# Kernel tuning notes

Hardware: AMD Instinct MI355X
Metric: run time of the kernel (lower is better)

## Reference

```python
import jax, jax.numpy as jnp
import numpy as np

W = 5           # input_instances
H = W // 2      # half_input_instances
N = 16384       # total ragged tokens (sum of lengths)
D = 1024        # hidden_dim


def setup_inputs() -> dict:
    key = jax.random.key(0)
    # 8 variable-length sequences summing to N
    lengths = np.array([1024, 3072, 2048, 4096, 512, 1536, 2560, 1536], dtype=np.int64)
    assert lengths.sum() == N
    x = jax.random.normal(key, (N, D), dtype=jnp.float32)
    return {"x": x, "lengths": jnp.asarray(lengths)}


def reference(x, lengths):
    # Equivalent to: per-sequence zero-pad by H on both sides, unfold window W stride 1,
    # concat, reshape to [N, D*W]. out[n, d*W + w] = padded_seq[t + w, d] where t is the
    # local position of token n, zero when t + w - H is out of the sequence.
    n, d = x.shape
    cum = jnp.cumsum(lengths)                 # [S] sequence end offsets
    starts = cum - lengths                    # [S] sequence start offsets
    pos = jnp.arange(n)                       # [N] global token index
    seg = jnp.searchsorted(cum, pos, side='right')  # [N] sequence id per token
    local = pos - starts[seg]                 # [N] local position within sequence
    seq_len = lengths[seg]                    # [N] length of owning sequence
    offs = jnp.arange(W) - H                  # [W] window offsets relative to center
    src_local = local[:, None] + offs[None, :]              # [N, W]
    valid = (src_local >= 0) & (src_local < seq_len[:, None])
    src = jnp.clip(src_local, 0, seq_len[:, None] - 1) + starts[seg][:, None]
    gathered = jnp.where(valid[:, :, None], x[src], jnp.zeros((), x.dtype))  # [N, W, D]
    # unfold layout is [N, D, W]; row-major flatten -> out[n, d*W + w]
    return jnp.transpose(gathered, (0, 2, 1)).reshape(n, d * W)
```

## Files before the change

kernel.cpp:

```cpp
#include <hip/hip_runtime.h>


#define WIN 5
#define HALF 2
#define DIM 1024
#define DV (DIM / 4)
#define OUTV (DV * WIN)
#define NSEQ 8
#define T 8
#define ROWS (T + 2 * HALF)

typedef float f32x4 __attribute__((ext_vector_type(4)));

__global__ __launch_bounds__(256) void inflate_kernel(
    const f32x4* __restrict__ x4,
    const int*   __restrict__ lengths,
    f32x4*       __restrict__ out4,
    int N)
{
    __shared__ float lds[ROWS * DIM];

    const int nb    = gridDim.x;
    const int chunk = nb >> 3;
    const int bid   = blockIdx.x;
    const int newb  = (bid & 7) * chunk + (bid >> 3);
    const int t0    = newb * T;

    const int g = threadIdx.x;

    f32x4* lds4 = (f32x4*)lds;
#pragma unroll
    for (int rr = 0; rr < ROWS; ++rr) {
        const int gr = t0 - HALF + rr;
        f32x4 v = (f32x4)0.f;
        if (gr >= 0 && gr < N) v = x4[(size_t)gr * DV + g];
        lds4[rr * DV + g] = v;
    }

    int Ls[NSEQ];
#pragma unroll
    for (int s = 0; s < NSEQ; ++s) Ls[s] = lengths[s];

    __syncthreads();

    const int wid  = g >> 6;
    const int lane = g & 63;

#pragma unroll
    for (int ti = 0; ti < 2; ++ti) {
        const int tt = wid * 2 + ti;
        const int n  = t0 + tt;

        int start = 0, end = N, acc = 0;
#pragma unroll
        for (int s = 0; s < NSEQ; ++s) {
            const int L = Ls[s];
            if (n >= acc && n < acc + L) { start = acc; end = acc + L; }
            acc += L;
        }
        int wlo = start - n + HALF; if (wlo < 0) wlo = 0;
        int whi = end - n + HALF - 1; if (whi > WIN - 1) whi = WIN - 1;

        const float* ldsbase = lds + tt * DIM;
        f32x4* dst = out4 + (size_t)n * OUTV;

        if (wlo == 0 && whi == WIN - 1) {
#pragma unroll
            for (int k = 0; k < OUTV / 64; ++k) {
                const unsigned j  = k * 64 + lane;
                const unsigned p0 = 4 * j;
                f32x4 o;
                { unsigned p = p0 + 0, d = p / WIN, w = p - d * WIN; o.x = ldsbase[w * DIM + d]; }
                { unsigned p = p0 + 1, d = p / WIN, w = p - d * WIN; o.y = ldsbase[w * DIM + d]; }
                { unsigned p = p0 + 2, d = p / WIN, w = p - d * WIN; o.z = ldsbase[w * DIM + d]; }
                { unsigned p = p0 + 3, d = p / WIN, w = p - d * WIN; o.w = ldsbase[w * DIM + d]; }
                __builtin_nontemporal_store(o, &dst[j]);
            }
        } else {
#pragma unroll
            for (int k = 0; k < OUTV / 64; ++k) {
                const unsigned j  = k * 64 + lane;
                const unsigned p0 = 4 * j;
                f32x4 o;
                { unsigned p = p0 + 0, d = p / WIN; int w = (int)(p - d * WIN);
                  o.x = (w >= wlo && w <= whi) ? ldsbase[w * DIM + d] : 0.f; }
                { unsigned p = p0 + 1, d = p / WIN; int w = (int)(p - d * WIN);
                  o.y = (w >= wlo && w <= whi) ? ldsbase[w * DIM + d] : 0.f; }
                { unsigned p = p0 + 2, d = p / WIN; int w = (int)(p - d * WIN);
                  o.z = (w >= wlo && w <= whi) ? ldsbase[w * DIM + d] : 0.f; }
                { unsigned p = p0 + 3, d = p / WIN; int w = (int)(p - d * WIN);
                  o.w = (w >= wlo && w <= whi) ? ldsbase[w * DIM + d] : 0.f; }
                __builtin_nontemporal_store(o, &dst[j]);
            }
        }
    }
}

extern "C" void kernel_launch(void* const* d_in, const int* in_sizes, int n_in,
                              void* d_out, int out_size, void* d_ws, size_t ws_size,
                              hipStream_t stream) {
    const float* x       = (const float*)d_in[0];
    const int*   lengths = (const int*)d_in[1];
    float*       out     = (float*)d_out;

    const int N = in_sizes[0] / DIM;

    dim3 grid(N / T), block(256);
    hipLaunchKernelGGL(inflate_kernel, grid, block, 0, stream,
                       (const f32x4*)x, lengths, (f32x4*)out, N);
}
```

Baseline: 72.28 us.

## Double token tile, split hidden dim in halves, load LDS via global_load_lds

Raises the tokens per block from 8 to 16, which shrinks the halo re-read overhead from 12/8 to 20/16 rows per block. To keep LDS size bounded, the hidden dimension is processed in two halves with a barrier between them. Input rows are loaded straight into LDS with the global_load_lds builtin, bypassing registers. Each wave now emits four output rows per half. The trade-off is half as many blocks, an extra synchronisation point, and no overlap between loading the second half and storing the first.

```diff
diff --git a/kernel.cpp b/kernel.cpp
--- a/kernel.cpp
+++ b/kernel.cpp
@@ -7,18 +7,27 @@
 #define DV (DIM / 4)
 #define OUTV (DV * WIN)
 #define NSEQ 8
-#define T 8
+#define T 16
 #define ROWS (T + 2 * HALF)
+#define HD (DIM / 2)
+#define HOUTV (OUTV / 2)
 
 typedef float f32x4 __attribute__((ext_vector_type(4)));
 
+__device__ inline void gload_lds16(const float* g, float* l) {
+    __builtin_amdgcn_global_load_lds(
+        (const __attribute__((address_space(1))) void*)g,
+        (__attribute__((address_space(3))) void*)l,
+        16, 0, 0);
+}
+
 __global__ __launch_bounds__(256) void inflate_kernel(
-    const f32x4* __restrict__ x4,
+    const float* __restrict__ x,
     const int*   __restrict__ lengths,
     f32x4*       __restrict__ out4,
     int N)
 {
-    __shared__ float lds[ROWS * DIM];
+    __shared__ float lds[ROWS * HD];
 
     const int nb    = gridDim.x;
     const int chunk = nb >> 3;
@@ -26,71 +35,84 @@
     const int newb  = (bid & 7) * chunk + (bid >> 3);
     const int t0    = newb * T;
 
-    const int g = threadIdx.x;
-
-    f32x4* lds4 = (f32x4*)lds;
-#pragma unroll
-    for (int rr = 0; rr < ROWS; ++rr) {
-        const int gr = t0 - HALF + rr;
-        f32x4 v = (f32x4)0.f;
-        if (gr >= 0 && gr < N) v = x4[(size_t)gr * DV + g];
-        lds4[rr * DV + g] = v;
-    }
+    const int g    = threadIdx.x;
+    const int wid  = g >> 6;
+    const int lane = g & 63;
 
     int Ls[NSEQ];
 #pragma unroll
     for (int s = 0; s < NSEQ; ++s) Ls[s] = lengths[s];
 
-    __syncthreads();
-
-    const int wid  = g >> 6;
-    const int lane = g & 63;
+#pragma unroll
+    for (int hp = 0; hp < 2; ++hp) {
+        if (hp) __syncthreads();
 
 #pragma unroll
-    for (int ti = 0; ti < 2; ++ti) {
-        const int tt = wid * 2 + ti;
-        const int n  = t0 + tt;
+        for (int i = 0; i < (ROWS * 2) / 4; ++i) {
+            const int c   = i * 4 + wid;
+            const int rr  = c >> 1;
+            const int sub = c & 1;
+            const int gr  = t0 - HALF + rr;
+            float* lbase = lds + rr * HD + sub * 256;
+            if (gr >= 0 && gr < N) {
+                const float* gsrc = x + (size_t)gr * DIM + hp * HD
+                                      + sub * 256 + lane * 4;
+                gload_lds16(gsrc, lbase);
+            } else {
+                *(f32x4*)(lbase + lane * 4) = (f32x4)0.f;
+            }
+        }
+        __syncthreads();
 
-        int start = 0, end = N, acc = 0;
 #pragma unroll
-        for (int s = 0; s < NSEQ; ++s) {
-            const int L = Ls[s];
-            if (n >= acc && n < acc + L) { start = acc; end = acc + L; }
-            acc += L;
-        }
-        int wlo = start - n + HALF; if (wlo < 0) wlo = 0;
-        int whi = end - n + HALF - 1; if (whi > WIN - 1) whi = WIN - 1;
+        for (int ti = 0; ti < 4; ++ti) {
+            const int tt = wid * 4 + ti;
+            const int n  = t0 + tt;
 
-        const float* ldsbase = lds + tt * DIM;
-        f32x4* dst = out4 + (size_t)n * OUTV;
+            int start = 0, end = N, acc = 0;
+#pragma unroll
+            for (int s = 0; s < NSEQ; ++s) {
+                const int L = Ls[s];
+                if (n >= acc && n < acc + L) { start = acc; end = acc + L; }
+                acc += L;
+            }
+            int wlo = start - n + HALF; if (wlo < 0) wlo = 0;
+            int whi = end - n + HALF - 1; if (whi > WIN - 1) whi = WIN - 1;
 
-        if (wlo == 0 && whi == WIN - 1) {
+            f32x4* dst = out4 + (size_t)n * OUTV + hp * HOUTV;
+
+            if (wlo == 0 && whi == WIN - 1) {
 #pragma unroll
-            for (int k = 0; k < OUTV / 64; ++k) {
-                const unsigned j  = k * 64 + lane;
-                const unsigned p0 = 4 * j;
-                f32x4 o;
-                { unsigned p = p0 + 0, d = p / WIN, w = p - d * WIN; o.x = ldsbase[w * DIM + d]; }
-                { unsigned p = p0 + 1, d = p / WIN, w = p - d * WIN; o.y = ldsbase[w * DIM + d]; }
-                { unsigned p = p0 + 2, d = p / WIN, w = p - d * WIN; o.z = ldsbase[w * DIM + d]; }
-                { unsigned p = p0 + 3, d = p / WIN, w = p - d * WIN; o.w = ldsbase[w * DIM + d]; }
-                __builtin_nontemporal_store(o, &dst[j]);
-            }
-        } else {
+                for (int k = 0; k < HOUTV / 64; ++k) {
+                    const unsigned jl = k * 64 + lane;
+                    const unsigned pg = hp * (HOUTV * 4) + 4 * jl;
+                    f32x4 o;
+                    { unsigned p = pg + 0, d = p / WIN, w = p - WIN * d;
+                      o.x = lds[(tt + w) * HD + (d - hp * HD)]; }
+                    { unsigned p = pg + 1, d = p / WIN, w = p - WIN * d;
+                      o.y = lds[(tt + w) * HD + (d - hp * HD)]; }
+                    { unsigned p = pg + 2, d = p / WIN, w = p - WIN * d;
+                      o.z = lds[(tt + w) * HD + (d - hp * HD)]; }
+                    { unsigned p = pg + 3, d = p / WIN, w = p - WIN * d;
+                      o.w = lds[(tt + w) * HD + (d - hp * HD)]; }
+                    __builtin_nontemporal_store(o, &dst[jl]);
+                }
+            } else {
 #pragma unroll
-            for (int k = 0; k < OUTV / 64; ++k) {
-                const unsigned j  = k * 64 + lane;
-                const unsigned p0 = 4 * j;
-                f32x4 o;
-                { unsigned p = p0 + 0, d = p / WIN; int w = (int)(p - d * WIN);
-                  o.x = (w >= wlo && w <= whi) ? ldsbase[w * DIM + d] : 0.f; }
-                { unsigned p = p0 + 1, d = p / WIN; int w = (int)(p - d * WIN);
-                  o.y = (w >= wlo && w <= whi) ? ldsbase[w * DIM + d] : 0.f; }
-                { unsigned p = p0 + 2, d = p / WIN; int w = (int)(p - d * WIN);
-                  o.z = (w >= wlo && w <= whi) ? ldsbase[w * DIM + d] : 0.f; }
-                { unsigned p = p0 + 3, d = p / WIN; int w = (int)(p - d * WIN);
-                  o.w = (w >= wlo && w <= whi) ? ldsbase[w * DIM + d] : 0.f; }
-                __builtin_nontemporal_store(o, &dst[j]);
+                for (int k = 0; k < HOUTV / 64; ++k) {
+                    const unsigned jl = k * 64 + lane;
+                    const unsigned pg = hp * (HOUTV * 4) + 4 * jl;
+                    f32x4 o;
+                    { unsigned p = pg + 0, d = p / WIN; int w = (int)(p - WIN * d);
+                      o.x = (w >= wlo && w <= whi) ? lds[(tt + w) * HD + (d - hp * HD)] : 0.f; }
+                    { unsigned p = pg + 1, d = p / WIN; int w = (int)(p - WIN * d);
+                      o.y = (w >= wlo && w <= whi) ? lds[(tt + w) * HD + (d - hp * HD)] : 0.f; }
+                    { unsigned p = pg + 2, d = p / WIN; int w = (int)(p - WIN * d);
+                      o.z = (w >= wlo && w <= whi) ? lds[(tt + w) * HD + (d - hp * HD)] : 0.f; }
+                    { unsigned p = pg + 3, d = p / WIN; int w = (int)(p - WIN * d);
+                      o.w = (w >= wlo && w <= whi) ? lds[(tt + w) * HD + (d - hp * HD)] : 0.f; }
+                    __builtin_nontemporal_store(o, &dst[jl]);
+                }
             }
         }
     }
@@ -107,5 +129,5 @@
 
     dim3 grid(N / T), block(256);
     hipLaunchKernelGGL(inflate_kernel, grid, block, 0, stream,
-                       (const f32x4*)x, lengths, (f32x4*)out, N);
+                       x, lengths, (f32x4*)out, N);
 }
```

New measurement: 74.83 us. +3.5%, slower.
